# Kernel tuning notes

Measured on AMD Instinct MI355X. Metric: run time of the kernel, lower is better.

The kernel has to match this reference:

```python
import jax, jax.numpy as jnp
import numpy as np

N = 100000   # points in input set
K = 1024     # num centroids AND max neighbors per ball (as in original code)
C = 64       # input feature channels
R = 0.2      # ball radius
LAYERS = (64, 64, 128)


def setup_inputs() -> dict:
    key = jax.random.key(0)
    ks = jax.random.split(key, 9)
    coords = jax.random.uniform(ks[0], (N, 3), dtype=jnp.float32)
    features = jax.random.normal(ks[1], (N, C), dtype=jnp.float32)
    centroid_idx = jax.random.randint(ks[2], (K,), 0, N)
    dims = (3 + C,) + LAYERS
    params = {}
    for i in range(len(LAYERS)):
        fin, fout = dims[i], dims[i + 1]
        params[f"W{i+1}"] = (jax.random.normal(ks[3 + i], (fin, fout), dtype=jnp.float32)
                             / np.float32(np.sqrt(fin)))
        params[f"b{i+1}"] = jax.random.normal(ks[6 + i], (fout,), dtype=jnp.float32) * 0.01
    return dict(coords=coords, features=features, centroid_idx=centroid_idx, **params)


def reference(coords, features, centroid_idx, W1, b1, W2, b2, W3, b3):
    cent = coords[centroid_idx]                                   # [K,3]
    # squared distances [K,N] without materializing [K,N,3]
    d2 = (jnp.sum(cent * cent, axis=-1)[:, None]
          + jnp.sum(coords * coords, axis=-1)[None, :]
          - 2.0 * cent @ coords.T)
    mask = d2 <= R * R                                            # ball query
    # take the FIRST K in-radius points in original index order (matches [:K])
    rank = jnp.cumsum(mask.astype(jnp.int32), axis=1) - 1
    sel = mask & (rank < K)
    order = jnp.where(sel, jnp.arange(N)[None, :], N)
    idx = jnp.sort(order, axis=1)[:, :K]                          # [K,K]
    valid = idx < N
    idx_c = jnp.minimum(idx, N - 1)
    rel = coords[idx_c] - cent[:, None, :]                        # centered coords
    x = jnp.concatenate([rel, features[idx_c]], axis=-1)          # [K,K,3+C]
    for W, b in ((W1, b1), (W2, b2), (W3, b3)):
        x = jax.nn.relu(x @ W + b)
    x = jnp.where(valid[:, :, None], x, -jnp.inf)
    new_features = jnp.max(x, axis=1)                             # per-region max pool
    return cent, new_features
```

## Files before the change

### kernel.cpp

```cpp
#include <hip/hip_runtime.h>
#include <hip/hip_bf16.h>

#define NPTS    100000
#define KCENT   1024
#define NSEG    391
#define NWORDS  1564
#define MB_BLKS (NSEG*64)

typedef __attribute__((ext_vector_type(8))) short bf16x8;
typedef __attribute__((ext_vector_type(4))) float f32x4;
typedef unsigned long long u64;

__device__ __forceinline__ unsigned short f2bf(float x) {
  union { float f; unsigned u; } v; v.f = x;
  unsigned r = v.u + 0x7FFFu + ((v.u >> 16) & 1u);
  return (unsigned short)(r >> 16);
}
__device__ __forceinline__ unsigned pk2bf(float a, float b) {
  union { __hip_bfloat162 h; unsigned u; } cv;
  cv.h = __float22bfloat162_rn(make_float2(a, b));
  return cv.u;
}
__device__ __forceinline__ bf16x8 pack_bf8(f32x4 a, f32x4 b) {
  union { bf16x8 v; unsigned u[4]; } r;
  r.u[0] = pk2bf(a[0], a[1]); r.u[1] = pk2bf(a[2], a[3]);
  r.u[2] = pk2bf(b[0], b[1]); r.u[3] = pk2bf(b[2], b[3]);
  return r.v;
}

__global__ __launch_bounds__(256) void build_prep_kernel(
    const float* __restrict__ coords, const float* __restrict__ features,
    const int* __restrict__ cidx, const float* __restrict__ W1,
    const float* __restrict__ b1, const float* __restrict__ W2,
    const float* __restrict__ W3, u64* __restrict__ maskbuf,
    unsigned short* __restrict__ featsBF, f32x4* __restrict__ coords4,
    unsigned short* __restrict__ W1T, unsigned short* __restrict__ W2T,
    unsigned short* __restrict__ W3T, float* __restrict__ outCent) {
  const int bid = blockIdx.x;
  const int tid = threadIdx.x;
  if (bid < MB_BLKS) {
    const int grp = bid / NSEG, seg = bid - grp*NSEG;
    __shared__ u64 sWords[64];
    const int lane = tid & 63, wid = tid >> 6;
    float cx[16], cy[16], cz[16], cc[16];
    #pragma unroll
    for (int j = 0; j < 16; ++j) {
      int c = cidx[grp*16 + j];
      cx[j] = coords[c*3]; cy[j] = coords[c*3+1]; cz[j] = coords[c*3+2];
      cc[j] = __fadd_rn(__fadd_rn(__fmul_rn(cx[j],cx[j]), __fmul_rn(cy[j],cy[j])),
                        __fmul_rn(cz[j],cz[j]));
    }
    const int p = seg*256 + tid;
    const bool inr = p < NPTS;
    float px = 0.f, py = 0.f, pz = 0.f;
    if (inr) { px = coords[p*3]; py = coords[p*3+1]; pz = coords[p*3+2]; }
    const float pp = __fadd_rn(__fadd_rn(__fmul_rn(px,px), __fmul_rn(py,py)),
                               __fmul_rn(pz,pz));
    u64 myw = 0ull;
    #pragma unroll
    for (int ci = 0; ci < 16; ++ci) {
      float dt = __fadd_rn(__fadd_rn(__fmul_rn(cx[ci],px), __fmul_rn(cy[ci],py)),
                           __fmul_rn(cz[ci],pz));
      float d2 = __fsub_rn(__fadd_rn(cc[ci], pp), __fmul_rn(2.0f, dt));
      bool sel = inr && (d2 <= 0.04f);
      u64 m = __ballot(sel);
      if (lane == ci) myw = m;
    }
    if (lane < 16) sWords[wid*16 + lane] = myw;
    __syncthreads();
    if (tid < 64) {
      int wwid = tid >> 4, ci = tid & 15;
      maskbuf[(u64)(seg*4 + wwid)*1024 + grp*16 + ci] = sWords[wwid*16 + ci];
    }
    return;
  }
  int i = (bid - MB_BLKS) * 256 + tid;
  if (i < 800000) {
    const f32x4* src = (const f32x4*)features + i*2;
    f32x4 f0 = src[0], f1 = src[1];
    union { bf16x8 v; uint4 u; } pk; pk.v = pack_bf8(f0, f1);
    ((uint4*)featsBF)[i] = pk.u;
    return;
  }
  i -= 800000;
  if (i < NPTS) {
    coords4[i] = (f32x4){coords[3*i], coords[3*i+1], coords[3*i+2], 0.f};
    return;
  }
  i -= NPTS;
  if (i < 6144) {
    int n = i / 96, kk = i - n*96;
    float v = 0.f;
    if (kk < 64)       v = W1[(3+kk)*64 + n];
    else if (kk < 67)  v = W1[(kk-64)*64 + n];
    else if (kk == 67) v = b1[n];
    W1T[n*96 + kk] = f2bf(v);
    return;
  }
  i -= 6144;
  if (i < 4608) { int n = i / 72, kk = i - n*72;
    W2T[n*72 + kk] = f2bf(kk < 64 ? W2[kk*64 + n] : 0.f); return; }
  i -= 4608;
  if (i < 9216) { int n = i / 72, kk = i - n*72;
    W3T[n*72 + kk] = f2bf(kk < 64 ? W3[kk*128 + n] : 0.f); return; }
  i -= 9216;
  if (i < KCENT) {
    int ci = cidx[i];
    outCent[i*3+0] = coords[ci*3+0];
    outCent[i*3+1] = coords[ci*3+1];
    outCent[i*3+2] = coords[ci*3+2];
  }
}

__global__ __launch_bounds__(256, 2) void fused_kernel(
    const u64* __restrict__ maskbuf, const unsigned short* __restrict__ featsBF,
    const f32x4* __restrict__ coords4, const float* __restrict__ cent,
    const float* __restrict__ b2v, const float* __restrict__ b3v,
    const unsigned short* __restrict__ gW1T, const unsigned short* __restrict__ gW2T,
    const unsigned short* __restrict__ gW3T, float* __restrict__ outF) {
  __shared__ __align__(16) unsigned short sW2T[64*72];
  __shared__ __align__(16) unsigned short sH[4*2*16*72];
  __shared__ int sIdx[KCENT];
  __shared__ int sTot[4];
  __shared__ float sB2[64], sB3[128];
  __shared__ float sMax[512];

  const int k = blockIdx.x;
  const int tid = threadIdx.x;
  const int w = tid >> 6, lane = tid & 63;
  const int q = lane >> 4, cl = lane & 15;

  u64 wv0 = maskbuf[(u64)tid*1024 + k];
  u64 wv1 = maskbuf[(u64)(256 + tid)*1024 + k];
  u64 wv2 = maskbuf[(u64)(512 + tid)*1024 + k];

  for (int i = tid; i < 576; i += 256) ((uint4*)sW2T)[i] = ((const uint4*)gW2T)[i];
  if (tid < 64)  sB2[tid] = b2v[tid];
  if (tid < 128) sB3[tid] = b3v[tid];

  bf16x8 w1f[3][4], w3f[2][8];
  #pragma unroll
  for (int ks = 0; ks < 3; ++ks)
    #pragma unroll
    for (int nt = 0; nt < 4; ++nt)
      w1f[ks][nt] = *(const bf16x8*)(gW1T + (nt*16+cl)*96 + ks*32 + q*8);
  #pragma unroll
  for (int ks = 0; ks < 2; ++ks)
    #pragma unroll
    for (int nt = 0; nt < 8; ++nt)
      w3f[ks][nt] = *(const bf16x8*)(gW3T + (nt*16+cl)*72 + ks*32 + q*8);

  int base = 0;
  #pragma unroll 1
  for (int r = 0; r < 7; ++r) {
    const int widx = r*256 + tid;
    u64 word = (r == 0) ? wv0 : (r == 1) ? wv1 : (r == 2) ? wv2
             : ((widx < NWORDS) ? maskbuf[(u64)widx*1024 + k] : 0ull);
    int pc = __popcll(word);
    int inc = pc;
    #pragma unroll
    for (int d = 1; d < 64; d <<= 1) {
      int t = __shfl_up(inc, d);
      if (lane >= d) inc += t;
    }
    if (lane == 63) sTot[w] = inc;
    __syncthreads();
    int wbase = 0, tot = 0;
    #pragma unroll
    for (int i = 0; i < 4; ++i) { int v = sTot[i]; tot += v; if (i < w) wbase += v; }
    int pos = base + wbase + inc - pc;
    const int pbase = widx * 64;
    while (word != 0ull && pos < KCENT) {
      int b = __ffsll(word) - 1;
      sIdx[pos++] = pbase + b;
      word &= word - 1ull;
    }
    base += tot;
    __syncthreads();
    if (base >= KCENT) break;
  }
  const int count = base < KCENT ? base : KCENT;

  const float cx = cent[k*3], cy = cent[k*3+1], cz = cent[k*3+2];
  unsigned short* myHA = sH + w*2304;
  unsigned short* myHB = myHA + 1152;

  f32x4 runmax[8];
  #pragma unroll
  for (int i = 0; i < 8; ++i)
    runmax[i] = (f32x4){-__builtin_inff(), -__builtin_inff(),
                        -__builtin_inff(), -__builtin_inff()};

  const int nstrips = (count + 15) >> 4;
  const int npairs  = (nstrips + 1) >> 1;
  int pp = w;

  int pA = 0, pB = 0;
  { int jA = 32*pp + cl;      if (jA < count) pA = sIdx[jA];
    int jB = 32*pp + 16 + cl; if (jB < count) pB = sIdx[jB]; }
  f32x4  c4A = coords4[pA], c4B = coords4[pB];
  bf16x8 xfA0 = *(const bf16x8*)(featsBF + pA*64 + q*8);
  bf16x8 xfA1 = *(const bf16x8*)(featsBF + pA*64 + 32 + q*8);
  bf16x8 xfB0 = *(const bf16x8*)(featsBF + pB*64 + q*8);
  bf16x8 xfB1 = *(const bf16x8*)(featsBF + pB*64 + 32 + q*8);
  int pA2 = 0, pB2 = 0;
  { int jA = 32*(pp+4) + cl;      if (jA < count) pA2 = sIdx[jA];
    int jB = 32*(pp+4) + 16 + cl; if (jB < count) pB2 = sIdx[jB]; }

  const bf16x8 zero8 = (bf16x8){0,0,0,0,0,0,0,0};

  for (; pp < npairs; pp += 4) {
    int pA3 = 0, pB3 = 0;
    { int jA = 32*(pp+8) + cl;      if (jA < count) pA3 = sIdx[jA];
      int jB = 32*(pp+8) + 16 + cl; if (jB < count) pB3 = sIdx[jB]; }

    union { bf16x8 v; unsigned u[4]; } rfA, rfB;
    rfA.u[0] = pk2bf(c4A[0]-cx, c4A[1]-cy); rfA.u[1] = pk2bf(c4A[2]-cz, 1.0f);
    rfA.u[2] = 0u; rfA.u[3] = 0u;
    rfB.u[0] = pk2bf(c4B[0]-cx, c4B[1]-cy); rfB.u[1] = pk2bf(c4B[2]-cz, 1.0f);
    rfB.u[2] = 0u; rfB.u[3] = 0u;
    bf16x8 x2A = (q == 0) ? rfA.v : zero8;
    bf16x8 x2B = (q == 0) ? rfB.v : zero8;

    {
      f32x4 accA[4], accB[4];
      #pragma unroll
      for (int nt = 0; nt < 4; ++nt) { accA[nt] = (f32x4){0.f,0.f,0.f,0.f};
                                       accB[nt] = (f32x4){0.f,0.f,0.f,0.f}; }
      #pragma unroll
      for (int nt = 0; nt < 4; ++nt) {
        accA[nt] = __builtin_amdgcn_mfma_f32_16x16x32_bf16(w1f[0][nt], xfA0, accA[nt], 0,0,0);
        accB[nt] = __builtin_amdgcn_mfma_f32_16x16x32_bf16(w1f[0][nt], xfB0, accB[nt], 0,0,0);
      }
      #pragma unroll
      for (int nt = 0; nt < 4; ++nt) {
        accA[nt] = __builtin_amdgcn_mfma_f32_16x16x32_bf16(w1f[1][nt], xfA1, accA[nt], 0,0,0);
        accB[nt] = __builtin_amdgcn_mfma_f32_16x16x32_bf16(w1f[1][nt], xfB1, accB[nt], 0,0,0);
      }
      #pragma unroll
      for (int nt = 0; nt < 4; ++nt) {
        accA[nt] = __builtin_amdgcn_mfma_f32_16x16x32_bf16(w1f[2][nt], x2A, accA[nt], 0,0,0);
        accB[nt] = __builtin_amdgcn_mfma_f32_16x16x32_bf16(w1f[2][nt], x2B, accB[nt], 0,0,0);
      }
      #pragma unroll
      for (int nt = 0; nt < 4; ++nt) {
        const int o = nt*16 + q*4;
        uint2 pkA = { pk2bf(fmaxf(accA[nt][0],0.f), fmaxf(accA[nt][1],0.f)),
                      pk2bf(fmaxf(accA[nt][2],0.f), fmaxf(accA[nt][3],0.f)) };
        *(uint2*)(myHA + cl*72 + o) = pkA;
        uint2 pkB = { pk2bf(fmaxf(accB[nt][0],0.f), fmaxf(accB[nt][1],0.f)),
                      pk2bf(fmaxf(accB[nt][2],0.f), fmaxf(accB[nt][3],0.f)) };
        *(uint2*)(myHB + cl*72 + o) = pkB;
      }
    }

    c4A = coords4[pA2]; c4B = coords4[pB2];
    xfA0 = *(const bf16x8*)(featsBF + pA2*64 + q*8);
    xfA1 = *(const bf16x8*)(featsBF + pA2*64 + 32 + q*8);
    xfB0 = *(const bf16x8*)(featsBF + pB2*64 + q*8);
    xfB1 = *(const bf16x8*)(featsBF + pB2*64 + 32 + q*8);

    {
      bf16x8 hA0 = *(const bf16x8*)(myHA + cl*72 + q*8);
      bf16x8 hA1 = *(const bf16x8*)(myHA + cl*72 + 32 + q*8);
      bf16x8 hB0 = *(const bf16x8*)(myHB + cl*72 + q*8);
      bf16x8 hB1 = *(const bf16x8*)(myHB + cl*72 + 32 + q*8);
      f32x4 accA[4], accB[4];
      #pragma unroll
      for (int nt = 0; nt < 4; ++nt) { accA[nt] = (f32x4){0.f,0.f,0.f,0.f};
                                       accB[nt] = (f32x4){0.f,0.f,0.f,0.f}; }
      #pragma unroll
      for (int nt = 0; nt < 4; ++nt) {
        const unsigned short* wrow = sW2T + (nt*16+cl)*72 + q*8;
        bf16x8 wa0 = *(const bf16x8*)(wrow);
        accA[nt] = __builtin_amdgcn_mfma_f32_16x16x32_bf16(wa0, hA0, accA[nt], 0,0,0);
        accB[nt] = __builtin_amdgcn_mfma_f32_16x16x32_bf16(wa0, hB0, accB[nt], 0,0,0);
        bf16x8 wa1 = *(const bf16x8*)(wrow + 32);
        accA[nt] = __builtin_amdgcn_mfma_f32_16x16x32_bf16(wa1, hA1, accA[nt], 0,0,0);
        accB[nt] = __builtin_amdgcn_mfma_f32_16x16x32_bf16(wa1, hB1, accB[nt], 0,0,0);
      }
      #pragma unroll
      for (int nt = 0; nt < 4; ++nt) {
        const int o = nt*16 + q*4;
        f32x4 bb = *(const f32x4*)(sB2 + o);
        uint2 pkA = { pk2bf(fmaxf(accA[nt][0]+bb[0],0.f), fmaxf(accA[nt][1]+bb[1],0.f)),
                      pk2bf(fmaxf(accA[nt][2]+bb[2],0.f), fmaxf(accA[nt][3]+bb[3],0.f)) };
        *(uint2*)(myHA + cl*72 + o) = pkA;
        uint2 pkB = { pk2bf(fmaxf(accB[nt][0]+bb[0],0.f), fmaxf(accB[nt][1]+bb[1],0.f)),
                      pk2bf(fmaxf(accB[nt][2]+bb[2],0.f), fmaxf(accB[nt][3]+bb[3],0.f)) };
        *(uint2*)(myHB + cl*72 + o) = pkB;
      }
    }

    {
      bf16x8 hA0 = *(const bf16x8*)(myHA + cl*72 + q*8);
      bf16x8 hA1 = *(const bf16x8*)(myHA + cl*72 + 32 + q*8);
      bf16x8 hB0 = *(const bf16x8*)(myHB + cl*72 + q*8);
      bf16x8 hB1 = *(const bf16x8*)(myHB + cl*72 + 32 + q*8);
      const float vmA = (32*pp + cl      < count) ? 0.f : -__builtin_inff();
      const float vmB = (32*pp + 16 + cl < count) ? 0.f : -__builtin_inff();
      f32x4 a3A[8], a3B[8];
      #pragma unroll
      for (int nt = 0; nt < 8; ++nt) { a3A[nt] = (f32x4){0.f,0.f,0.f,0.f};
                                       a3B[nt] = (f32x4){0.f,0.f,0.f,0.f}; }
      #pragma unroll
      for (int nt = 0; nt < 8; ++nt) {
        a3A[nt] = __builtin_amdgcn_mfma_f32_16x16x32_bf16(w3f[0][nt], hA0, a3A[nt], 0,0,0);
        a3B[nt] = __builtin_amdgcn_mfma_f32_16x16x32_bf16(w3f[0][nt], hB0, a3B[nt], 0,0,0);
      }
      #pragma unroll
      for (int nt = 0; nt < 8; ++nt) {
        a3A[nt] = __builtin_amdgcn_mfma_f32_16x16x32_bf16(w3f[1][nt], hA1, a3A[nt], 0,0,0);
        a3B[nt] = __builtin_amdgcn_mfma_f32_16x16x32_bf16(w3f[1][nt], hB1, a3B[nt], 0,0,0);
      }
      #pragma unroll
      for (int nt = 0; nt < 8; ++nt)
        #pragma unroll
        for (int r = 0; r < 4; ++r)
          runmax[nt][r] = fmaxf(runmax[nt][r],
                                fmaxf(a3A[nt][r] + vmA, a3B[nt][r] + vmB));
    }

    pA2 = pA3; pB2 = pB3;
  }

  #pragma unroll
  for (int nt = 0; nt < 8; ++nt) {
    #pragma unroll
    for (int r = 0; r < 4; ++r) {
      float m = runmax[nt][r];
      m = fmaxf(m, __shfl_xor(m, 1));
      m = fmaxf(m, __shfl_xor(m, 2));
      m = fmaxf(m, __shfl_xor(m, 4));
      m = fmaxf(m, __shfl_xor(m, 8));
      runmax[nt][r] = m;
    }
    if (cl == 0) *(f32x4*)(sMax + w*128 + nt*16 + q*4) = runmax[nt];
  }
  __syncthreads();
  if (tid < 128) {
    float m = fmaxf(fmaxf(sMax[tid], sMax[128+tid]),
                    fmaxf(sMax[256+tid], sMax[384+tid]));
    outF[k*128 + tid] = fmaxf(m + sB3[tid], 0.f);
  }
}

extern "C" void kernel_launch(void* const* d_in, const int* in_sizes, int n_in,
                              void* d_out, int out_size, void* d_ws, size_t ws_size,
                              hipStream_t stream) {
  const float* coords   = (const float*)d_in[0];
  const float* features = (const float*)d_in[1];
  const int*   cidx     = (const int*)d_in[2];
  const float* W1 = (const float*)d_in[3];
  const float* b1 = (const float*)d_in[4];
  const float* W2 = (const float*)d_in[5];
  const float* b2 = (const float*)d_in[6];
  const float* W3 = (const float*)d_in[7];
  const float* b3 = (const float*)d_in[8];
  float* out = (float*)d_out;

  char* ws = (char*)d_ws;
  u64* maskbuf            = (u64*)(ws + 0);
  unsigned short* featsBF = (unsigned short*)(ws + 13107200);
  f32x4* coords4          = (f32x4*)(ws + 25907200);
  unsigned short* W1T = (unsigned short*)(ws + 27507200);
  unsigned short* W2T = (unsigned short*)(ws + 27519488);
  unsigned short* W3T = (unsigned short*)(ws + 27528704);

  build_prep_kernel<<<MB_BLKS + 3598, 256, 0, stream>>>(
      coords, features, cidx, W1, b1, W2, W3,
      maskbuf, featsBF, coords4, W1T, W2T, W3T, out);
  fused_kernel<<<KCENT, 256, 0, stream>>>(
      maskbuf, featsBF, coords4, out, b2, b3,
      W1T, W2T, W3T, out + 3072);
}
```

Before: 226.2 us.

## Replace precomputed ball-query bitmask with per-centroid on-the-fly scan and early exit

Drops the global K×N bitmask build from the prep kernel. Each centroid block now computes distances to points in chunks of 1024, compacts hits with ballot/popcount prefix sums, and stops once K neighbours are found. This removes the full all-pairs distance pass and the 13 MB mask write and read. In exchange, every block streams point coordinates repeatedly from L2, and blocks with sparse neighbourhoods scan further.

```diff
diff --git a/kernel.cpp b/kernel.cpp
--- a/kernel.cpp
+++ b/kernel.cpp
@@ -3,9 +3,6 @@
 
 #define NPTS    100000
 #define KCENT   1024
-#define NSEG    391
-#define NWORDS  1564
-#define MB_BLKS (NSEG*64)
 
 typedef __attribute__((ext_vector_type(8))) short bf16x8;
 typedef __attribute__((ext_vector_type(4))) float f32x4;
@@ -28,53 +25,15 @@
   return r.v;
 }
 
-__global__ __launch_bounds__(256) void build_prep_kernel(
+__global__ __launch_bounds__(256) void prep_kernel(
     const float* __restrict__ coords, const float* __restrict__ features,
     const int* __restrict__ cidx, const float* __restrict__ W1,
     const float* __restrict__ b1, const float* __restrict__ W2,
-    const float* __restrict__ W3, u64* __restrict__ maskbuf,
+    const float* __restrict__ W3,
     unsigned short* __restrict__ featsBF, f32x4* __restrict__ coords4,
     unsigned short* __restrict__ W1T, unsigned short* __restrict__ W2T,
     unsigned short* __restrict__ W3T, float* __restrict__ outCent) {
-  const int bid = blockIdx.x;
-  const int tid = threadIdx.x;
-  if (bid < MB_BLKS) {
-    const int grp = bid / NSEG, seg = bid - grp*NSEG;
-    __shared__ u64 sWords[64];
-    const int lane = tid & 63, wid = tid >> 6;
-    float cx[16], cy[16], cz[16], cc[16];
-    #pragma unroll
-    for (int j = 0; j < 16; ++j) {
-      int c = cidx[grp*16 + j];
-      cx[j] = coords[c*3]; cy[j] = coords[c*3+1]; cz[j] = coords[c*3+2];
-      cc[j] = __fadd_rn(__fadd_rn(__fmul_rn(cx[j],cx[j]), __fmul_rn(cy[j],cy[j])),
-                        __fmul_rn(cz[j],cz[j]));
-    }
-    const int p = seg*256 + tid;
-    const bool inr = p < NPTS;
-    float px = 0.f, py = 0.f, pz = 0.f;
-    if (inr) { px = coords[p*3]; py = coords[p*3+1]; pz = coords[p*3+2]; }
-    const float pp = __fadd_rn(__fadd_rn(__fmul_rn(px,px), __fmul_rn(py,py)),
-                               __fmul_rn(pz,pz));
-    u64 myw = 0ull;
-    #pragma unroll
-    for (int ci = 0; ci < 16; ++ci) {
-      float dt = __fadd_rn(__fadd_rn(__fmul_rn(cx[ci],px), __fmul_rn(cy[ci],py)),
-                           __fmul_rn(cz[ci],pz));
-      float d2 = __fsub_rn(__fadd_rn(cc[ci], pp), __fmul_rn(2.0f, dt));
-      bool sel = inr && (d2 <= 0.04f);
-      u64 m = __ballot(sel);
-      if (lane == ci) myw = m;
-    }
-    if (lane < 16) sWords[wid*16 + lane] = myw;
-    __syncthreads();
-    if (tid < 64) {
-      int wwid = tid >> 4, ci = tid & 15;
-      maskbuf[(u64)(seg*4 + wwid)*1024 + grp*16 + ci] = sWords[wwid*16 + ci];
-    }
-    return;
-  }
-  int i = (bid - MB_BLKS) * 256 + tid;
+  int i = blockIdx.x * 256 + threadIdx.x;
   if (i < 800000) {
     const f32x4* src = (const f32x4*)features + i*2;
     f32x4 f0 = src[0], f1 = src[1];
@@ -113,15 +72,15 @@
 }
 
 __global__ __launch_bounds__(256, 2) void fused_kernel(
-    const u64* __restrict__ maskbuf, const unsigned short* __restrict__ featsBF,
-    const f32x4* __restrict__ coords4, const float* __restrict__ cent,
-    const float* __restrict__ b2v, const float* __restrict__ b3v,
-    const unsigned short* __restrict__ gW1T, const unsigned short* __restrict__ gW2T,
-    const unsigned short* __restrict__ gW3T, float* __restrict__ outF) {
+    const unsigned short* __restrict__ featsBF, const f32x4* __restrict__ coords4,
+    const float* __restrict__ cent, const float* __restrict__ b2v,
+    const float* __restrict__ b3v, const unsigned short* __restrict__ gW1T,
+    const unsigned short* __restrict__ gW2T, const unsigned short* __restrict__ gW3T,
+    float* __restrict__ outF) {
   __shared__ __align__(16) unsigned short sW2T[64*72];
   __shared__ __align__(16) unsigned short sH[4*2*16*72];
   __shared__ int sIdx[KCENT];
-  __shared__ int sTot[4];
+  __shared__ __align__(16) int sTot[16];
   __shared__ float sB2[64], sB3[128];
   __shared__ float sMax[512];
 
@@ -130,10 +89,6 @@
   const int w = tid >> 6, lane = tid & 63;
   const int q = lane >> 4, cl = lane & 15;
 
-  u64 wv0 = maskbuf[(u64)tid*1024 + k];
-  u64 wv1 = maskbuf[(u64)(256 + tid)*1024 + k];
-  u64 wv2 = maskbuf[(u64)(512 + tid)*1024 + k];
-
   for (int i = tid; i < 576; i += 256) ((uint4*)sW2T)[i] = ((const uint4*)gW2T)[i];
   if (tid < 64)  sB2[tid] = b2v[tid];
   if (tid < 128) sB3[tid] = b3v[tid];
@@ -150,38 +105,70 @@
     for (int nt = 0; nt < 8; ++nt)
       w3f[ks][nt] = *(const bf16x8*)(gW3T + (nt*16+cl)*72 + ks*32 + q*8);
 
+  const float cx = cent[k*3], cy = cent[k*3+1], cz = cent[k*3+2];
+  const float cc = __fadd_rn(__fadd_rn(__fmul_rn(cx,cx), __fmul_rn(cy,cy)),
+                             __fmul_rn(cz,cz));
+
   int base = 0;
+  f32x4 pc[4];
+  #pragma unroll
+  for (int j = 0; j < 4; ++j) {
+    int p = j*256 + tid;
+    pc[j] = (p < NPTS) ? coords4[p] : (f32x4){1e9f, 1e9f, 1e9f, 0.f};
+  }
+  const u64 ltmask = (1ull << lane) - 1ull;
   #pragma unroll 1
-  for (int r = 0; r < 7; ++r) {
-    const int widx = r*256 + tid;
-    u64 word = (r == 0) ? wv0 : (r == 1) ? wv1 : (r == 2) ? wv2
-             : ((widx < NWORDS) ? maskbuf[(u64)widx*1024 + k] : 0ull);
-    int pc = __popcll(word);
-    int inc = pc;
-    #pragma unroll
-    for (int d = 1; d < 64; d <<= 1) {
-      int t = __shfl_up(inc, d);
-      if (lane >= d) inc += t;
-    }
-    if (lane == 63) sTot[w] = inc;
+  for (int rb = 0; rb < 98; ++rb) {
+    f32x4 pcn[4];
+    if (rb + 1 < 98) {
+      #pragma unroll
+      for (int j = 0; j < 4; ++j) {
+        int p = (rb+1)*1024 + j*256 + tid;
+        pcn[j] = (p < NPTS) ? coords4[p] : (f32x4){1e9f, 1e9f, 1e9f, 0.f};
+      }
+    }
+    u64 wds[4];
+    #pragma unroll
+    for (int j = 0; j < 4; ++j) {
+      float px = pc[j][0], py = pc[j][1], pz = pc[j][2];
+      float pp = __fadd_rn(__fadd_rn(__fmul_rn(px,px), __fmul_rn(py,py)),
+                           __fmul_rn(pz,pz));
+      float dt = __fadd_rn(__fadd_rn(__fmul_rn(cx,px), __fmul_rn(cy,py)),
+                           __fmul_rn(cz,pz));
+      float d2 = __fsub_rn(__fadd_rn(cc, pp), __fmul_rn(2.0f, dt));
+      int p = rb*1024 + j*256 + tid;
+      bool sel = (p < NPTS) && (d2 <= 0.04f);
+      wds[j] = __ballot(sel);
+    }
+    if (lane == 0) {
+      sTot[     w] = __popcll(wds[0]);
+      sTot[ 4 + w] = __popcll(wds[1]);
+      sTot[ 8 + w] = __popcll(wds[2]);
+      sTot[12 + w] = __popcll(wds[3]);
+    }
     __syncthreads();
-    int wbase = 0, tot = 0;
-    #pragma unroll
-    for (int i = 0; i < 4; ++i) { int v = sTot[i]; tot += v; if (i < w) wbase += v; }
-    int pos = base + wbase + inc - pc;
-    const int pbase = widx * 64;
-    while (word != 0ull && pos < KCENT) {
-      int b = __ffsll(word) - 1;
-      sIdx[pos++] = pbase + b;
-      word &= word - 1ull;
-    }
-    base += tot;
+    int4 t0 = *(const int4*)(sTot);
+    int4 t1 = *(const int4*)(sTot + 4);
+    int4 t2 = *(const int4*)(sTot + 8);
+    int4 t3 = *(const int4*)(sTot + 12);
+    int tv[16] = {t0.x,t0.y,t0.z,t0.w, t1.x,t1.y,t1.z,t1.w,
+                  t2.x,t2.y,t2.z,t2.w, t3.x,t3.y,t3.z,t3.w};
+    int pre[16]; int run = 0;
+    #pragma unroll
+    for (int i = 0; i < 16; ++i) { pre[i] = run; run += tv[i]; }
+    #pragma unroll
+    for (int j = 0; j < 4; ++j) {
+      int pos = base + pre[j*4 + w] + __popcll(wds[j] & ltmask);
+      bool mine = (wds[j] >> lane) & 1ull;
+      if (mine && pos < KCENT) sIdx[pos] = rb*1024 + j*256 + tid;
+    }
+    base += run;
     __syncthreads();
     if (base >= KCENT) break;
+    pc[0] = pcn[0]; pc[1] = pcn[1]; pc[2] = pcn[2]; pc[3] = pcn[3];
   }
   const int count = base < KCENT ? base : KCENT;
 
-  const float cx = cent[k*3], cy = cent[k*3+1], cz = cent[k*3+2];
   unsigned short* myHA = sH + w*2304;
   unsigned short* myHB = myHA + 1152;
 
@@ -360,17 +347,16 @@
   float* out = (float*)d_out;
 
   char* ws = (char*)d_ws;
-  u64* maskbuf            = (u64*)(ws + 0);
-  unsigned short* featsBF = (unsigned short*)(ws + 13107200);
-  f32x4* coords4          = (f32x4*)(ws + 25907200);
-  unsigned short* W1T = (unsigned short*)(ws + 27507200);
-  unsigned short* W2T = (unsigned short*)(ws + 27519488);
-  unsigned short* W3T = (unsigned short*)(ws + 27528704);
-
-  build_prep_kernel<<<MB_BLKS + 3598, 256, 0, stream>>>(
+  unsigned short* featsBF = (unsigned short*)(ws + 0);
+  f32x4* coords4          = (f32x4*)(ws + 12800000);
+  unsigned short* W1T = (unsigned short*)(ws + 14400000);
+  unsigned short* W2T = (unsigned short*)(ws + 14412288);
+  unsigned short* W3T = (unsigned short*)(ws + 14421504);
+
+  prep_kernel<<<3598, 256, 0, stream>>>(
       coords, features, cidx, W1, b1, W2, W3,
-      maskbuf, featsBF, coords4, W1T, W2T, W3T, out);
+      featsBF, coords4, W1T, W2T, W3T, out);
   fused_kernel<<<KCENT, 256, 0, stream>>>(
-      maskbuf, featsBF, coords4, out, b2, b3,
+      featsBF, coords4, out, b2, b3,
       W1T, W2T, W3T, out + 3072);
 }
```

After: 360.2 us. 59.2% more time.
